# Optimization experiments

Measured on AMD Instinct MI355X. Metric: run time of the kernel, lower is better.

The kernel has to match this reference:

```python
import jax, jax.numpy as jnp
from jax import lax
import numpy as np

B, T, H, K = 128, 256, 768, 64


def setup_inputs() -> dict:
    key = jax.random.key(0)
    k1, k2, k3, k4 = jax.random.split(key, 4)
    hidden = jax.random.normal(k1, (B, T, H), dtype=jnp.float32)
    masks = jnp.ones((B, T), dtype=jnp.int32)
    target = jax.random.randint(k2, (B, T), 0, K, dtype=jnp.int32)
    W = jax.random.normal(k3, (H, K), dtype=jnp.float32) * 0.02
    b = jnp.zeros((K,), dtype=jnp.float32)
    transitions = jax.random.uniform(k4, (K, K), dtype=jnp.float32)
    return {"hidden": hidden, "masks": masks, "target": target,
            "W": W, "b": b, "transitions": transitions}


def _crf_log_norm(emissions, trans, seq_len):
    # emissions: [B,T,K]; forward algorithm (log-sum-exp recurrence over time)
    Tn = emissions.shape[1]
    alpha0 = emissions[:, 0]  # [B,K]

    def step(alpha, xs):
        emis_t, t = xs
        new = jax.nn.logsumexp(alpha[:, :, None] + trans[None], axis=1) + emis_t
        alpha = jnp.where((t < seq_len)[:, None], new, alpha)
        return alpha, None

    xs = (jnp.swapaxes(emissions[:, 1:], 0, 1), jnp.arange(1, Tn))
    alpha, _ = lax.scan(step, alpha0, xs)
    return jax.nn.logsumexp(alpha, axis=1)  # [B]


def _crf_sequence_score(emissions, tags, trans, seq_len):
    Tn = emissions.shape[1]
    t_idx = jnp.arange(Tn)
    valid = t_idx[None, :] < seq_len[:, None]  # [B,T]
    unary = jnp.take_along_axis(emissions, tags[..., None], axis=2)[..., 0]
    unary = jnp.sum(jnp.where(valid, unary, 0.0), axis=1)
    pair = trans[tags[:, :-1], tags[:, 1:]]  # [B,T-1]
    valid_pair = t_idx[1:][None, :] < seq_len[:, None]
    binary = jnp.sum(jnp.where(valid_pair, pair, 0.0), axis=1)
    return unary + binary


def _crf_decode(emissions, trans, seq_len):
    # Viterbi with backpointers; padded steps carry state (identity backptr)
    Bn, Tn, Kn = emissions.shape
    v0 = emissions[:, 0]

    def step(v, xs):
        emis_t, t = xs
        scores = v[:, :, None] + trans[None]  # [B, K_prev, K_cur]
        bp = jnp.argmax(scores, axis=1).astype(jnp.int32)
        new_v = jnp.max(scores, axis=1) + emis_t
        m = (t < seq_len)[:, None]
        v = jnp.where(m, new_v, v)
        bp = jnp.where(m, bp, jnp.arange(Kn, dtype=jnp.int32)[None])
        return v, bp

    xs = (jnp.swapaxes(emissions[:, 1:], 0, 1), jnp.arange(1, Tn))
    v, bps = lax.scan(step, v0, xs)  # bps: [T-1, B, K]
    best_score = jnp.max(v, axis=1)
    last_tag = jnp.argmax(v, axis=1).astype(jnp.int32)

    def back(tag, bp_t):
        prev = jnp.take_along_axis(bp_t, tag[:, None], axis=1)[:, 0]
        return prev, prev

    _, rev_tags = lax.scan(back, last_tag, bps, reverse=True)  # [T-1, B]
    path = jnp.concatenate([rev_tags, last_tag[None]], axis=0)  # [T, B]
    path = jnp.swapaxes(path, 0, 1)  # [B, T]
    valid = jnp.arange(Tn)[None, :] < seq_len[:, None]
    path = jnp.where(valid, path, 0)
    return path, best_score


def reference(hidden, masks, target, W, b, transitions):
    # dense projection (dropout omitted for determinism)
    emissions = jnp.einsum('bth,hk->btk', hidden, W) + b  # [B,T,K]
    seq_len = jnp.sum(masks, axis=1).astype(jnp.int32)
    log_norm = _crf_log_norm(emissions, transitions, seq_len)
    seq_score = _crf_sequence_score(emissions, target, transitions, seq_len)
    log_likelihood = seq_score - log_norm  # [B]
    decode_predict, _crf_scores = _crf_decode(emissions, transitions, seq_len)
    return decode_predict, log_likelihood
```

## Files before the change

### kernel.cpp

```cpp
#include <hip/hip_runtime.h>

#define B_ 128
#define T_ 256
#define H_ 768
#define K_ 64
#define BT_ (B_ * T_)

template <int CTRL>
__device__ __forceinline__ float dpp_mov_f(float x) {
    return __int_as_float(__builtin_amdgcn_update_dpp(
        __float_as_int(x), __float_as_int(x), CTRL, 0xF, 0xF, false));
}
__device__ __forceinline__ float wave_max64(float x) {
    x = fmaxf(x, dpp_mov_f<0x111>(x));
    x = fmaxf(x, dpp_mov_f<0x112>(x));
    x = fmaxf(x, dpp_mov_f<0x114>(x));
    x = fmaxf(x, dpp_mov_f<0x118>(x));
    x = fmaxf(x, dpp_mov_f<0x142>(x));
    x = fmaxf(x, dpp_mov_f<0x143>(x));
    return __int_as_float(__builtin_amdgcn_readlane(__float_as_int(x), 63));
}
__device__ __forceinline__ float readlane0_f(float x) {
    return __int_as_float(__builtin_amdgcn_readfirstlane(__float_as_int(x)));
}
template <int I>
__device__ __forceinline__ float readlane_f(float x) {
    return __int_as_float(__builtin_amdgcn_readlane(__float_as_int(x), I));
}

#define BK_ 32
#define P_ 130
__global__ __launch_bounds__(256) void gemm_emis(const float* __restrict__ hidden,
                                                 const float* __restrict__ W,
                                                 const float* __restrict__ bias,
                                                 float* __restrict__ emis) {
    __shared__ float At[BK_ * P_];

    const int tid = threadIdx.x;
    const int lane = tid & 63;
    const int wc = __builtin_amdgcn_readfirstlane((tid >> 6) * 16);
    const int rowbase = blockIdx.x * 128;
    const int srow = tid >> 3;
    const int sh4 = tid & 7;

    float acc0[16], acc1[16];
#pragma unroll
    for (int c = 0; c < 16; ++c) { acc0[c] = bias[wc + c]; acc1[c] = acc0[c]; }

    float4 pf[4];
#pragma unroll
    for (int i = 0; i < 4; ++i)
        pf[i] = *(const float4*)&hidden[(rowbase + srow + i * 32) * H_ + sh4 * 4];

    for (int kb = 0; kb < H_ / BK_; ++kb) {
        __syncthreads();
#pragma unroll
        for (int i = 0; i < 4; ++i) {
            int row = srow + i * 32;
            At[(sh4 * 4 + 0) * P_ + row] = pf[i].x;
            At[(sh4 * 4 + 1) * P_ + row] = pf[i].y;
            At[(sh4 * 4 + 2) * P_ + row] = pf[i].z;
            At[(sh4 * 4 + 3) * P_ + row] = pf[i].w;
        }
        __syncthreads();
        if (kb + 1 < H_ / BK_) {
#pragma unroll
            for (int i = 0; i < 4; ++i)
                pf[i] = *(const float4*)&hidden[(rowbase + srow + i * 32) * H_ +
                                                (kb + 1) * BK_ + sh4 * 4];
        }
        const float* Wk = &W[(kb * BK_) * K_ + wc];
#pragma unroll 8
        for (int h = 0; h < BK_; ++h) {
            float2 a = *(const float2*)&At[h * P_ + 2 * lane];
            float4 w0 = *(const float4*)&Wk[h * K_ + 0];
            float4 w1 = *(const float4*)&Wk[h * K_ + 4];
            float4 w2 = *(const float4*)&Wk[h * K_ + 8];
            float4 w3 = *(const float4*)&Wk[h * K_ + 12];
            acc0[0]  += a.x * w0.x; acc1[0]  += a.y * w0.x;
            acc0[1]  += a.x * w0.y; acc1[1]  += a.y * w0.y;
            acc0[2]  += a.x * w0.z; acc1[2]  += a.y * w0.z;
            acc0[3]  += a.x * w0.w; acc1[3]  += a.y * w0.w;
            acc0[4]  += a.x * w1.x; acc1[4]  += a.y * w1.x;
            acc0[5]  += a.x * w1.y; acc1[5]  += a.y * w1.y;
            acc0[6]  += a.x * w1.z; acc1[6]  += a.y * w1.z;
            acc0[7]  += a.x * w1.w; acc1[7]  += a.y * w1.w;
            acc0[8]  += a.x * w2.x; acc1[8]  += a.y * w2.x;
            acc0[9]  += a.x * w2.y; acc1[9]  += a.y * w2.y;
            acc0[10] += a.x * w2.z; acc1[10] += a.y * w2.z;
            acc0[11] += a.x * w2.w; acc1[11] += a.y * w2.w;
            acc0[12] += a.x * w3.x; acc1[12] += a.y * w3.x;
            acc0[13] += a.x * w3.y; acc1[13] += a.y * w3.y;
            acc0[14] += a.x * w3.z; acc1[14] += a.y * w3.z;
            acc0[15] += a.x * w3.w; acc1[15] += a.y * w3.w;
        }
    }

    float* e0 = &emis[(size_t)(rowbase + 2 * lane) * K_ + wc];
    float* e1 = &emis[(size_t)(rowbase + 2 * lane + 1) * K_ + wc];
#pragma unroll
    for (int q = 0; q < 4; ++q) {
        *(float4*)&e0[q * 4] = make_float4(acc0[q * 4], acc0[q * 4 + 1],
                                           acc0[q * 4 + 2], acc0[q * 4 + 3]);
        *(float4*)&e1[q * 4] = make_float4(acc1[q * 4], acc1[q * 4 + 1],
                                           acc1[q * 4 + 2], acc1[q * 4 + 3]);
    }
}

__global__ __launch_bounds__(128, 1) void crf_kernel(const float* __restrict__ emis,
                                                     const int* __restrict__ masks,
                                                     const int* __restrict__ target,
                                                     const float* __restrict__ trans,
                                                     float* __restrict__ out) {
    __shared__ __align__(16) float ebuf[T_ * K_];
    __shared__ __align__(16) float vbuf[T_ * K_];
    __shared__ float tbuf[K_ * 65];

    const int tid = threadIdx.x;
    const int lane = tid & 63;
    const int b = blockIdx.x;
    const float* eb = emis + (size_t)b * (T_ * K_);

    {
        const float4* src = (const float4*)eb;
        float4* dst = (float4*)ebuf;
#pragma unroll
        for (int k = 0; k < 32; ++k) dst[tid + k * 128] = src[tid + k * 128];
    }
    int sl = 0;
#pragma unroll
    for (int k = 0; k < 4; ++k) sl += masks[b * T_ + lane + k * 64];
#pragma unroll
    for (int m = 32; m; m >>= 1) sl += __shfl_xor(sl, m, 64);
    const int seq_len = sl;
    __syncthreads();

    if (tid < 64) {
        float Ecol[64];
#pragma unroll
        for (int i = 0; i < 64; ++i) Ecol[i] = __expf(trans[i * K_ + lane]);

        float e_c = ebuf[lane];
        float e00 = readlane0_f(e_c);
        float p = __expf(e_c - e00);
        float C = e00;
        float logD0prev = 0.f;
        float e_n = ebuf[K_ + lane];
        float en0 = readlane0_f(e_n);
        float xg = __expf(e_n - en0);

        for (int t = 1; t < T_; ++t) {
            float e_f = (t < T_ - 1) ? ebuf[(t + 1) * K_ + lane] : 0.f;
            float a0 = 0.f, a1 = 0.f, a2 = 0.f, a3 = 0.f;
            float a4 = 0.f, a5 = 0.f, a6 = 0.f, a7 = 0.f;
#define FWD8(base)                                                     \
            a0 = fmaf(readlane_f<base + 0>(p), Ecol[base + 0], a0);    \
            a1 = fmaf(readlane_f<base + 1>(p), Ecol[base + 1], a1);    \
            a2 = fmaf(readlane_f<base + 2>(p), Ecol[base + 2], a2);    \
            a3 = fmaf(readlane_f<base + 3>(p), Ecol[base + 3], a3);    \
            a4 = fmaf(readlane_f<base + 4>(p), Ecol[base + 4], a4);    \
            a5 = fmaf(readlane_f<base + 5>(p), Ecol[base + 5], a5);    \
            a6 = fmaf(readlane_f<base + 6>(p), Ecol[base + 6], a6);    \
            a7 = fmaf(readlane_f<base + 7>(p), Ecol[base + 7], a7);
            FWD8(0) FWD8(8) FWD8(16) FWD8(24) FWD8(32) FWD8(40) FWD8(48) FWD8(56)
#undef FWD8
            float D = ((a0 + a1) + (a2 + a3)) + ((a4 + a5) + (a6 + a7));
            float pnew = D * xg;
            if (t < seq_len) { p = pnew; C += en0 + logD0prev; }
            float D0 = readlane0_f(D);
            logD0prev = __logf(D0);
            float gn = __fdividef(1.f, D0);
            en0 = readlane0_f(e_f);
            xg = __expf(e_f - en0) * gn;
            e_n = e_f;
        }
        float rs = p;
#pragma unroll
        for (int m = 32; m; m >>= 1) rs += __shfl_xor(rs, m, 64);
        float log_norm = C + __logf(rs);

        float sc = 0.f;
#pragma unroll
        for (int k = 0; k < 4; ++k) {
            int t = lane + k * 64;
            if (t < seq_len) {
                int tg = target[b * T_ + t];
                sc += ebuf[t * K_ + tg];
                if (t >= 1) sc += trans[target[b * T_ + t - 1] * K_ + tg];
            }
        }
#pragma unroll
        for (int m = 32; m; m >>= 1) sc += __shfl_xor(sc, m, 64);
        if (lane == 0) out[BT_ + b] = sc - log_norm;
    } else {
        float Tcol[64];
#pragma unroll
        for (int i = 0; i < 64; ++i) Tcol[i] = trans[i * K_ + lane];
        for (int idx = lane; idx < K_ * K_; idx += 64)
            tbuf[(idx >> 6) * 65 + (idx & 63)] = trans[idx];

        float v = ebuf[lane];
        vbuf[lane] = v;
        float e_n = ebuf[K_ + lane];
        for (int t = 1; t < T_; ++t) {
            float e_f = (t < T_ - 1) ? ebuf[(t + 1) * K_ + lane] : 0.f;
            float m0 = -3.4e38f, m1 = m0, m2 = m0, m3 = m0;
            float m4 = m0, m5 = m0, m6 = m0, m7 = m0;
#define VIT8(base)                                                        \
            m0 = fmaxf(m0, readlane_f<base + 0>(v) + Tcol[base + 0]);     \
            m1 = fmaxf(m1, readlane_f<base + 1>(v) + Tcol[base + 1]);     \
            m2 = fmaxf(m2, readlane_f<base + 2>(v) + Tcol[base + 2]);     \
            m3 = fmaxf(m3, readlane_f<base + 3>(v) + Tcol[base + 3]);     \
            m4 = fmaxf(m4, readlane_f<base + 4>(v) + Tcol[base + 4]);     \
            m5 = fmaxf(m5, readlane_f<base + 5>(v) + Tcol[base + 5]);     \
            m6 = fmaxf(m6, readlane_f<base + 6>(v) + Tcol[base + 6]);     \
            m7 = fmaxf(m7, readlane_f<base + 7>(v) + Tcol[base + 7]);
            VIT8(0) VIT8(8) VIT8(16) VIT8(24) VIT8(32) VIT8(40) VIT8(48) VIT8(56)
#undef VIT8
            float M = fmaxf(fmaxf(fmaxf(m0, m1), fmaxf(m2, m3)),
                            fmaxf(fmaxf(m4, m5), fmaxf(m6, m7)));
            float vn = M + e_n;
            if (t < seq_len) v = vn;
            vbuf[t * K_ + lane] = v;
            e_n = e_f;
        }

        float M = wave_max64(v);
        unsigned long long ball = __ballot(v >= M);
        int tag = (int)__builtin_ctzll(ball);

        int path[4];
#pragma unroll
        for (int k = 0; k < 4; ++k) path[k] = 0;
        if (lane == ((T_ - 1) & 63)) path[(T_ - 1) >> 6] = tag;

        float vpre = vbuf[(T_ - 2) * K_ + lane];
        for (int t = T_ - 1; t >= 1; --t) {
            float vnext = (t >= 2) ? vbuf[(t - 2) * K_ + lane] : 0.f;
            if (t < seq_len) {
                float s = vpre + tbuf[lane * 65 + tag];
                float Ms = wave_max64(s);
                unsigned long long bl = __ballot(s >= Ms);
                tag = (int)__builtin_ctzll(bl);
            }
            int pidx = t - 1;
            if (lane == (pidx & 63)) path[pidx >> 6] = tag;
            vpre = vnext;
        }
#pragma unroll
        for (int k = 0; k < 4; ++k) {
            int t = lane + k * 64;
            out[b * T_ + t] = (t < seq_len) ? (float)path[k] : 0.f;
        }
    }
}

extern "C" void kernel_launch(void* const* d_in, const int* in_sizes, int n_in,
                              void* d_out, int out_size, void* d_ws, size_t ws_size,
                              hipStream_t stream) {
    const float* hidden = (const float*)d_in[0];
    const int* masks    = (const int*)d_in[1];
    const int* target   = (const int*)d_in[2];
    const float* W      = (const float*)d_in[3];
    const float* bias   = (const float*)d_in[4];
    const float* trans  = (const float*)d_in[5];
    float* out = (float*)d_out;
    float* emis = (float*)d_ws;

    gemm_emis<<<dim3(BT_ / 128), dim3(256), 0, stream>>>(hidden, W, bias, emis);
    crf_kernel<<<dim3(B_), dim3(128), 0, stream>>>(emis, masks, target, trans, out);
}
```

Baseline: 378.3 us.

## Interleave two sequences per CRF block and widen GEMM to 512 threads

```diff
diff --git a/kernel.cpp b/kernel.cpp
--- a/kernel.cpp
+++ b/kernel.cpp
@@ -30,7 +30,7 @@
 
 #define BK_ 32
 #define P_ 130
-__global__ __launch_bounds__(256) void gemm_emis(const float* __restrict__ hidden,
+__global__ __launch_bounds__(512) void gemm_emis(const float* __restrict__ hidden,
                                                  const float* __restrict__ W,
                                                  const float* __restrict__ bias,
                                                  float* __restrict__ emis) {
@@ -38,36 +38,34 @@
 
     const int tid = threadIdx.x;
     const int lane = tid & 63;
-    const int wc = __builtin_amdgcn_readfirstlane((tid >> 6) * 16);
+    const int wc = __builtin_amdgcn_readfirstlane((tid >> 6) * 8);
     const int rowbase = blockIdx.x * 128;
-    const int srow = tid >> 3;
-    const int sh4 = tid & 7;
-
-    float acc0[16], acc1[16];
-#pragma unroll
-    for (int c = 0; c < 16; ++c) { acc0[c] = bias[wc + c]; acc1[c] = acc0[c]; }
-
-    float4 pf[4];
-#pragma unroll
-    for (int i = 0; i < 4; ++i)
-        pf[i] = *(const float4*)&hidden[(rowbase + srow + i * 32) * H_ + sh4 * 4];
+    const int srow = tid >> 2;
+    const int scol = (tid & 3) * 8;
+
+    float acc0[8], acc1[8];
+#pragma unroll
+    for (int c = 0; c < 8; ++c) { acc0[c] = bias[wc + c]; acc1[c] = acc0[c]; }
+
+    float4 pf0 = *(const float4*)&hidden[(size_t)(rowbase + srow) * H_ + scol];
+    float4 pf1 = *(const float4*)&hidden[(size_t)(rowbase + srow) * H_ + scol + 4];
 
     for (int kb = 0; kb < H_ / BK_; ++kb) {
         __syncthreads();
-#pragma unroll
-        for (int i = 0; i < 4; ++i) {
-            int row = srow + i * 32;
-            At[(sh4 * 4 + 0) * P_ + row] = pf[i].x;
-            At[(sh4 * 4 + 1) * P_ + row] = pf[i].y;
-            At[(sh4 * 4 + 2) * P_ + row] = pf[i].z;
-            At[(sh4 * 4 + 3) * P_ + row] = pf[i].w;
-        }
+        At[(scol + 0) * P_ + srow] = pf0.x;
+        At[(scol + 1) * P_ + srow] = pf0.y;
+        At[(scol + 2) * P_ + srow] = pf0.z;
+        At[(scol + 3) * P_ + srow] = pf0.w;
+        At[(scol + 4) * P_ + srow] = pf1.x;
+        At[(scol + 5) * P_ + srow] = pf1.y;
+        At[(scol + 6) * P_ + srow] = pf1.z;
+        At[(scol + 7) * P_ + srow] = pf1.w;
         __syncthreads();
         if (kb + 1 < H_ / BK_) {
-#pragma unroll
-            for (int i = 0; i < 4; ++i)
-                pf[i] = *(const float4*)&hidden[(rowbase + srow + i * 32) * H_ +
-                                                (kb + 1) * BK_ + sh4 * 4];
+            pf0 = *(const float4*)&hidden[(size_t)(rowbase + srow) * H_ +
+                                          (kb + 1) * BK_ + scol];
+            pf1 = *(const float4*)&hidden[(size_t)(rowbase + srow) * H_ +
+                                          (kb + 1) * BK_ + scol + 4];
         }
         const float* Wk = &W[(kb * BK_) * K_ + wc];
 #pragma unroll 8
@@ -75,36 +73,23 @@
             float2 a = *(const float2*)&At[h * P_ + 2 * lane];
             float4 w0 = *(const float4*)&Wk[h * K_ + 0];
             float4 w1 = *(const float4*)&Wk[h * K_ + 4];
-            float4 w2 = *(const float4*)&Wk[h * K_ + 8];
-            float4 w3 = *(const float4*)&Wk[h * K_ + 12];
-            acc0[0]  += a.x * w0.x; acc1[0]  += a.y * w0.x;
-            acc0[1]  += a.x * w0.y; acc1[1]  += a.y * w0.y;
-            acc0[2]  += a.x * w0.z; acc1[2]  += a.y * w0.z;
-            acc0[3]  += a.x * w0.w; acc1[3]  += a.y * w0.w;
-            acc0[4]  += a.x * w1.x; acc1[4]  += a.y * w1.x;
-            acc0[5]  += a.x * w1.y; acc1[5]  += a.y * w1.y;
-            acc0[6]  += a.x * w1.z; acc1[6]  += a.y * w1.z;
-            acc0[7]  += a.x * w1.w; acc1[7]  += a.y * w1.w;
-            acc0[8]  += a.x * w2.x; acc1[8]  += a.y * w2.x;
-            acc0[9]  += a.x * w2.y; acc1[9]  += a.y * w2.y;
-            acc0[10] += a.x * w2.z; acc1[10] += a.y * w2.z;
-            acc0[11] += a.x * w2.w; acc1[11] += a.y * w2.w;
-            acc0[12] += a.x * w3.x; acc1[12] += a.y * w3.x;
-            acc0[13] += a.x * w3.y; acc1[13] += a.y * w3.y;
-            acc0[14] += a.x * w3.z; acc1[14] += a.y * w3.z;
-            acc0[15] += a.x * w3.w; acc1[15] += a.y * w3.w;
+            acc0[0] += a.x * w0.x; acc1[0] += a.y * w0.x;
+            acc0[1] += a.x * w0.y; acc1[1] += a.y * w0.y;
+            acc0[2] += a.x * w0.z; acc1[2] += a.y * w0.z;
+            acc0[3] += a.x * w0.w; acc1[3] += a.y * w0.w;
+            acc0[4] += a.x * w1.x; acc1[4] += a.y * w1.x;
+            acc0[5] += a.x * w1.y; acc1[5] += a.y * w1.y;
+            acc0[6] += a.x * w1.z; acc1[6] += a.y * w1.z;
+            acc0[7] += a.x * w1.w; acc1[7] += a.y * w1.w;
         }
     }
 
     float* e0 = &emis[(size_t)(rowbase + 2 * lane) * K_ + wc];
     float* e1 = &emis[(size_t)(rowbase + 2 * lane + 1) * K_ + wc];
-#pragma unroll
-    for (int q = 0; q < 4; ++q) {
-        *(float4*)&e0[q * 4] = make_float4(acc0[q * 4], acc0[q * 4 + 1],
-                                           acc0[q * 4 + 2], acc0[q * 4 + 3]);
-        *(float4*)&e1[q * 4] = make_float4(acc1[q * 4], acc1[q * 4 + 1],
-                                           acc1[q * 4 + 2], acc1[q * 4 + 3]);
-    }
+    *(float4*)&e0[0] = make_float4(acc0[0], acc0[1], acc0[2], acc0[3]);
+    *(float4*)&e0[4] = make_float4(acc0[4], acc0[5], acc0[6], acc0[7]);
+    *(float4*)&e1[0] = make_float4(acc1[0], acc1[1], acc1[2], acc1[3]);
+    *(float4*)&e1[4] = make_float4(acc1[4], acc1[5], acc1[6], acc1[7]);
 }
 
 __global__ __launch_bounds__(128, 1) void crf_kernel(const float* __restrict__ emis,
@@ -112,86 +97,117 @@
                                                      const int* __restrict__ target,
                                                      const float* __restrict__ trans,
                                                      float* __restrict__ out) {
-    __shared__ __align__(16) float ebuf[T_ * K_];
-    __shared__ __align__(16) float vbuf[T_ * K_];
+    __shared__ __align__(16) float vbufA[T_ * K_];
+    __shared__ __align__(16) float vbufB[T_ * K_];
     __shared__ float tbuf[K_ * 65];
+    __shared__ int tagsA[T_];
+    __shared__ int tagsB[T_];
 
     const int tid = threadIdx.x;
     const int lane = tid & 63;
-    const int b = blockIdx.x;
-    const float* eb = emis + (size_t)b * (T_ * K_);
-
-    {
-        const float4* src = (const float4*)eb;
-        float4* dst = (float4*)ebuf;
-#pragma unroll
-        for (int k = 0; k < 32; ++k) dst[tid + k * 128] = src[tid + k * 128];
+    const int bA = blockIdx.x * 2;
+    const int bB = bA + 1;
+    const float* eA = emis + (size_t)bA * (T_ * K_);
+    const float* eB = emis + (size_t)bB * (T_ * K_);
+
+    int sa = 0, sb = 0;
+#pragma unroll
+    for (int k = 0; k < 4; ++k) {
+        sa += masks[bA * T_ + lane + k * 64];
+        sb += masks[bB * T_ + lane + k * 64];
     }
-    int sl = 0;
-#pragma unroll
-    for (int k = 0; k < 4; ++k) sl += masks[b * T_ + lane + k * 64];
-#pragma unroll
-    for (int m = 32; m; m >>= 1) sl += __shfl_xor(sl, m, 64);
-    const int seq_len = sl;
-    __syncthreads();
+#pragma unroll
+    for (int m = 32; m; m >>= 1) {
+        sa += __shfl_xor(sa, m, 64);
+        sb += __shfl_xor(sb, m, 64);
+    }
+    const int slA = sa, slB = sb;
 
     if (tid < 64) {
         float Ecol[64];
 #pragma unroll
         for (int i = 0; i < 64; ++i) Ecol[i] = __expf(trans[i * K_ + lane]);
 
-        float e_c = ebuf[lane];
-        float e00 = readlane0_f(e_c);
-        float p = __expf(e_c - e00);
-        float C = e00;
-        float logD0prev = 0.f;
-        float e_n = ebuf[K_ + lane];
-        float en0 = readlane0_f(e_n);
-        float xg = __expf(e_n - en0);
+        float ecA = eA[lane], ecB = eB[lane];
+        float CA = readlane0_f(ecA), CB = readlane0_f(ecB);
+        float pA = __expf(ecA - CA), pB = __expf(ecB - CB);
+        float lDA = 0.f, lDB = 0.f;
+        float enA = eA[K_ + lane], enB = eB[K_ + lane];
+        float e0A = readlane0_f(enA), e0B = readlane0_f(enB);
+        float xgA = __expf(enA - e0A), xgB = __expf(enB - e0B);
 
         for (int t = 1; t < T_; ++t) {
-            float e_f = (t < T_ - 1) ? ebuf[(t + 1) * K_ + lane] : 0.f;
+            float efA = (t < T_ - 1) ? eA[(t + 1) * K_ + lane] : 0.f;
+            float efB = (t < T_ - 1) ? eB[(t + 1) * K_ + lane] : 0.f;
             float a0 = 0.f, a1 = 0.f, a2 = 0.f, a3 = 0.f;
             float a4 = 0.f, a5 = 0.f, a6 = 0.f, a7 = 0.f;
-#define FWD8(base)                                                     \
-            a0 = fmaf(readlane_f<base + 0>(p), Ecol[base + 0], a0);    \
-            a1 = fmaf(readlane_f<base + 1>(p), Ecol[base + 1], a1);    \
-            a2 = fmaf(readlane_f<base + 2>(p), Ecol[base + 2], a2);    \
-            a3 = fmaf(readlane_f<base + 3>(p), Ecol[base + 3], a3);    \
-            a4 = fmaf(readlane_f<base + 4>(p), Ecol[base + 4], a4);    \
-            a5 = fmaf(readlane_f<base + 5>(p), Ecol[base + 5], a5);    \
-            a6 = fmaf(readlane_f<base + 6>(p), Ecol[base + 6], a6);    \
-            a7 = fmaf(readlane_f<base + 7>(p), Ecol[base + 7], a7);
+            float c0 = 0.f, c1 = 0.f, c2 = 0.f, c3 = 0.f;
+            float c4 = 0.f, c5 = 0.f, c6 = 0.f, c7 = 0.f;
+#define FWD8(base)                                                        \
+            a0 = fmaf(readlane_f<(base) + 0>(pA), Ecol[(base) + 0], a0);  \
+            c0 = fmaf(readlane_f<(base) + 0>(pB), Ecol[(base) + 0], c0);  \
+            a1 = fmaf(readlane_f<(base) + 1>(pA), Ecol[(base) + 1], a1);  \
+            c1 = fmaf(readlane_f<(base) + 1>(pB), Ecol[(base) + 1], c1);  \
+            a2 = fmaf(readlane_f<(base) + 2>(pA), Ecol[(base) + 2], a2);  \
+            c2 = fmaf(readlane_f<(base) + 2>(pB), Ecol[(base) + 2], c2);  \
+            a3 = fmaf(readlane_f<(base) + 3>(pA), Ecol[(base) + 3], a3);  \
+            c3 = fmaf(readlane_f<(base) + 3>(pB), Ecol[(base) + 3], c3);  \
+            a4 = fmaf(readlane_f<(base) + 4>(pA), Ecol[(base) + 4], a4);  \
+            c4 = fmaf(readlane_f<(base) + 4>(pB), Ecol[(base) + 4], c4);  \
+            a5 = fmaf(readlane_f<(base) + 5>(pA), Ecol[(base) + 5], a5);  \
+            c5 = fmaf(readlane_f<(base) + 5>(pB), Ecol[(base) + 5], c5);  \
+            a6 = fmaf(readlane_f<(base) + 6>(pA), Ecol[(base) + 6], a6);  \
+            c6 = fmaf(readlane_f<(base) + 6>(pB), Ecol[(base) + 6], c6);  \
+            a7 = fmaf(readlane_f<(base) + 7>(pA), Ecol[(base) + 7], a7);  \
+            c7 = fmaf(readlane_f<(base) + 7>(pB), Ecol[(base) + 7], c7);
             FWD8(0) FWD8(8) FWD8(16) FWD8(24) FWD8(32) FWD8(40) FWD8(48) FWD8(56)
 #undef FWD8
-            float D = ((a0 + a1) + (a2 + a3)) + ((a4 + a5) + (a6 + a7));
-            float pnew = D * xg;
-            if (t < seq_len) { p = pnew; C += en0 + logD0prev; }
-            float D0 = readlane0_f(D);
-            logD0prev = __logf(D0);
-            float gn = __fdividef(1.f, D0);
-            en0 = readlane0_f(e_f);
-            xg = __expf(e_f - en0) * gn;
-            e_n = e_f;
-        }
-        float rs = p;
-#pragma unroll
-        for (int m = 32; m; m >>= 1) rs += __shfl_xor(rs, m, 64);
-        float log_norm = C + __logf(rs);
-
-        float sc = 0.f;
+            float DA = ((a0 + a1) + (a2 + a3)) + ((a4 + a5) + (a6 + a7));
+            float DB = ((c0 + c1) + (c2 + c3)) + ((c4 + c5) + (c6 + c7));
+            float pnA = DA * xgA;
+            float pnB = DB * xgB;
+            if (t < slA) { pA = pnA; CA += e0A + lDA; }
+            if (t < slB) { pB = pnB; CB += e0B + lDB; }
+            float dA = readlane0_f(DA), dB = readlane0_f(DB);
+            lDA = __logf(dA); lDB = __logf(dB);
+            float gA = __fdividef(1.f, dA), gB = __fdividef(1.f, dB);
+            e0A = readlane0_f(efA); e0B = readlane0_f(efB);
+            xgA = __expf(efA - e0A) * gA;
+            xgB = __expf(efB - e0B) * gB;
+        }
+        float rsA = pA, rsB = pB;
+#pragma unroll
+        for (int m = 32; m; m >>= 1) {
+            rsA += __shfl_xor(rsA, m, 64);
+            rsB += __shfl_xor(rsB, m, 64);
+        }
+        float lnA = CA + __logf(rsA);
+        float lnB = CB + __logf(rsB);
+
+        float scA = 0.f, scB = 0.f;
 #pragma unroll
         for (int k = 0; k < 4; ++k) {
             int t = lane + k * 64;
-            if (t < seq_len) {
-                int tg = target[b * T_ + t];
-                sc += ebuf[t * K_ + tg];
-                if (t >= 1) sc += trans[target[b * T_ + t - 1] * K_ + tg];
+            if (t < slA) {
+                int tg = target[bA * T_ + t];
+                scA += eA[t * K_ + tg];
+                if (t >= 1) scA += trans[target[bA * T_ + t - 1] * K_ + tg];
             }
-        }
-#pragma unroll
-        for (int m = 32; m; m >>= 1) sc += __shfl_xor(sc, m, 64);
-        if (lane == 0) out[BT_ + b] = sc - log_norm;
+            if (t < slB) {
+                int tg = target[bB * T_ + t];
+                scB += eB[t * K_ + tg];
+                if (t >= 1) scB += trans[target[bB * T_ + t - 1] * K_ + tg];
+            }
+        }
+#pragma unroll
+        for (int m = 32; m; m >>= 1) {
+            scA += __shfl_xor(scA, m, 64);
+            scB += __shfl_xor(scB, m, 64);
+        }
+        if (lane == 0) {
+            out[BT_ + bA] = scA - lnA;
+            out[BT_ + bB] = scB - lnB;
+        }
     } else {
         float Tcol[64];
 #pragma unroll
@@ -199,58 +215,81 @@
         for (int idx = lane; idx < K_ * K_; idx += 64)
             tbuf[(idx >> 6) * 65 + (idx & 63)] = trans[idx];
 
-        float v = ebuf[lane];
-        vbuf[lane] = v;
-        float e_n = ebuf[K_ + lane];
+        float vA = eA[lane], vB = eB[lane];
+        vbufA[lane] = vA;
+        vbufB[lane] = vB;
+        float enA = eA[K_ + lane], enB = eB[K_ + lane];
+
         for (int t = 1; t < T_; ++t) {
-            float e_f = (t < T_ - 1) ? ebuf[(t + 1) * K_ + lane] : 0.f;
-            float m0 = -3.4e38f, m1 = m0, m2 = m0, m3 = m0;
-            float m4 = m0, m5 = m0, m6 = m0, m7 = m0;
+            float efA = (t < T_ - 1) ? eA[(t + 1) * K_ + lane] : 0.f;
+            float efB = (t < T_ - 1) ? eB[(t + 1) * K_ + lane] : 0.f;
+            float mA0 = -3.4e38f, mA1 = -3.4e38f, mA2 = -3.4e38f, mA3 = -3.4e38f;
+            float mB0 = -3.4e38f, mB1 = -3.4e38f, mB2 = -3.4e38f, mB3 = -3.4e38f;
+#define VITP(macc, vv, i0, i1)                                            \
+            {                                                             \
+                float x_ = readlane_f<(i0)>(vv) + Tcol[(i0)];             \
+                float y_ = readlane_f<(i1)>(vv) + Tcol[(i1)];             \
+                macc = fmaxf(fmaxf(macc, x_), y_);                        \
+            }
 #define VIT8(base)                                                        \
-            m0 = fmaxf(m0, readlane_f<base + 0>(v) + Tcol[base + 0]);     \
-            m1 = fmaxf(m1, readlane_f<base + 1>(v) + Tcol[base + 1]);     \
-            m2 = fmaxf(m2, readlane_f<base + 2>(v) + Tcol[base + 2]);     \
-            m3 = fmaxf(m3, readlane_f<base + 3>(v) + Tcol[base + 3]);     \
-            m4 = fmaxf(m4, readlane_f<base + 4>(v) + Tcol[base + 4]);     \
-            m5 = fmaxf(m5, readlane_f<base + 5>(v) + Tcol[base + 5]);     \
-            m6 = fmaxf(m6, readlane_f<base + 6>(v) + Tcol[base + 6]);     \
-            m7 = fmaxf(m7, readlane_f<base + 7>(v) + Tcol[base + 7]);
+            VITP(mA0, vA, (base) + 0, (base) + 1)                         \
+            VITP(mB0, vB, (base) + 0, (base) + 1)                         \
+            VITP(mA1, vA, (base) + 2, (base) + 3)                         \
+            VITP(mB1, vB, (base) + 2, (base) + 3)                         \
+            VITP(mA2, vA, (base) + 4, (base) + 5)                         \
+            VITP(mB2, vB, (base) + 4, (base) + 5)                         \
+            VITP(mA3, vA, (base) + 6, (base) + 7)                         \
+            VITP(mB3, vB, (base) + 6, (base) + 7)
             VIT8(0) VIT8(8) VIT8(16) VIT8(24) VIT8(32) VIT8(40) VIT8(48) VIT8(56)
 #undef VIT8
-            float M = fmaxf(fmaxf(fmaxf(m0, m1), fmaxf(m2, m3)),
-                            fmaxf(fmaxf(m4, m5), fmaxf(m6, m7)));
-            float vn = M + e_n;
-            if (t < seq_len) v = vn;
-            vbuf[t * K_ + lane] = v;
-            e_n = e_f;
-        }
-
-        float M = wave_max64(v);
-        unsigned long long ball = __ballot(v >= M);
-        int tag = (int)__builtin_ctzll(ball);
-
-        int path[4];
-#pragma unroll
-        for (int k = 0; k < 4; ++k) path[k] = 0;
-        if (lane == ((T_ - 1) & 63)) path[(T_ - 1) >> 6] = tag;
-
-        float vpre = vbuf[(T_ - 2) * K_ + lane];
-        for (int t = T_ - 1; t >= 1; --t) {
-            float vnext = (t >= 2) ? vbuf[(t - 2) * K_ + lane] : 0.f;
-            if (t < seq_len) {
-                float s = vpre + tbuf[lane * 65 + tag];
-                float Ms = wave_max64(s);
-                unsigned long long bl = __ballot(s >= Ms);
-                tag = (int)__builtin_ctzll(bl);
+#undef VITP
+            float MA = fmaxf(fmaxf(mA0, mA1), fmaxf(mA2, mA3));
+            float MB = fmaxf(fmaxf(mB0, mB1), fmaxf(mB2, mB3));
+            float vnA = MA + enA;
+            float vnB = MB + enB;
+            if (t < slA) vA = vnA;
+            if (t < slB) vB = vnB;
+            vbufA[t * K_ + lane] = vA;
+            vbufB[t * K_ + lane] = vB;
+            enA = efA; enB = efB;
+        }
+
+        {
+            float MA = wave_max64(vA);
+            unsigned long long blA = __ballot(vA >= MA);
+            int tgA = (int)__builtin_ctzll(blA);
+            float MB = wave_max64(vB);
+            unsigned long long blB = __ballot(vB >= MB);
+            int tgB = (int)__builtin_ctzll(blB);
+            if (lane == 0) { tagsA[T_ - 1] = tgA; tagsB[T_ - 1] = tgB; }
+
+            int tagA = tgA, tagB = tgB;
+            float vpA = vbufA[(T_ - 2) * K_ + lane];
+            float vpB = vbufB[(T_ - 2) * K_ + lane];
+            for (int t = T_ - 1; t >= 1; --t) {
+                float vxA = (t >= 2) ? vbufA[(t - 2) * K_ + lane] : 0.f;
+                float vxB = (t >= 2) ? vbufB[(t - 2) * K_ + lane] : 0.f;
+                if (t < slA) {
+                    float s = vpA + tbuf[lane * 65 + tagA];
+                    float Ms = wave_max64(s);
+                    unsigned long long bl = __ballot(s >= Ms);
+                    tagA = (int)__builtin_ctzll(bl);
+                }
+                if (t < slB) {
+                    float s = vpB + tbuf[lane * 65 + tagB];
+                    float Ms = wave_max64(s);
+                    unsigned long long bl = __ballot(s >= Ms);
+                    tagB = (int)__builtin_ctzll(bl);
+                }
+                if (lane == 0) { tagsA[t - 1] = tagA; tagsB[t - 1] = tagB; }
+                vpA = vxA; vpB = vxB;
             }
-            int pidx = t - 1;
-            if (lane == (pidx & 63)) path[pidx >> 6] = tag;
-            vpre = vnext;
         }
 #pragma unroll
         for (int k = 0; k < 4; ++k) {
             int t = lane + k * 64;
-            out[b * T_ + t] = (t < seq_len) ? (float)path[k] : 0.f;
+            out[bA * T_ + t] = (t < slA) ? (float)tagsA[t] : 0.f;
+            out[bB * T_ + t] = (t < slB) ? (float)tagsB[t] : 0.f;
         }
     }
 }
@@ -267,6 +306,6 @@
     float* out = (float*)d_out;
     float* emis = (float*)d_ws;
 
-    gemm_emis<<<dim3(BT_ / 128), dim3(256), 0, stream>>>(hidden, W, bias, emis);
-    crf_kernel<<<dim3(B_), dim3(128), 0, stream>>>(emis, masks, target, trans, out);
-}
+    gemm_emis<<<dim3(BT_ / 128), dim3(512), 0, stream>>>(hidden, W, bias, emis);
+    crf_kernel<<<dim3(B_ / 2), dim3(128), 0, stream>>>(emis, masks, target, trans, out);
+}
```

Result: slower. 557.6 us (+47.4%).
